# Performance work log

Hardware: AMD Instinct MI355X
Metric: run time of the kernel (lower is better)

The kernel has to match this reference:

```python
import jax, jax.numpy as jnp
import numpy as np

IN_FEATURES = 512
DIM_EXPLOSION = 20
OUT_FEATURES = IN_FEATURES * DIM_EXPLOSION  # 10240
NB_PROJ_ENTRIES = 6
HASH_LENGTH = 32
BATCH = 4096


def _make_sparse_proj(key):
    """Sparse binary random projection: each of the OUT_FEATURES rows has
    NB_PROJ_ENTRIES entries set to 1 (as in OlfactoryModel.create_rand_proj_matrix)."""
    idx = jax.random.randint(key, (OUT_FEATURES, NB_PROJ_ENTRIES), 0, IN_FEATURES)
    rows = jnp.arange(OUT_FEATURES)[:, None]
    W = jnp.zeros((OUT_FEATURES, IN_FEATURES), dtype=jnp.float32)
    return W.at[rows, idx].set(1.0)


def setup_inputs() -> dict:
    key = jax.random.key(0)
    k1, k2 = jax.random.split(key)
    inp = jax.random.uniform(k1, (BATCH, IN_FEATURES), dtype=jnp.float32)
    W = _make_sparse_proj(k2)
    return {"input": inp, "weight": W, "hash_length": HASH_LENGTH}


def reference(input, weight, hash_length):
    # F.linear: [B, in] @ [out, in]^T -> [B, out]
    x = jnp.einsum('bi,oi->bo', input, weight)
    # MB_sparsify: winner-take-all, keep top `hash_length` activations per row, zero the rest
    topv = jax.lax.top_k(x, hash_length)[0]          # [B, k]
    thresh = topv[:, -1:]                            # k-th largest per row
    return jnp.where(x >= thresh, x, jnp.zeros_like(x))
```

## Files before the change

kernel.cpp:

```cpp
#include <hip/hip_runtime.h>


typedef float f4 __attribute__((ext_vector_type(4)));

constexpr int IN_F   = 512;
constexpr int OUT_F  = 10240;
constexpr int TPB    = 1024;
constexpr int ROWS   = 4;
constexpr int FPT    = OUT_F / TPB;
constexpr int NBINS  = 1024;
constexpr int CHUNK  = 8;
constexpr int NCHUNK = NBINS / CHUNK;
constexpr int NWAVES = TPB / 64;
constexpr int CAP    = 64;

__global__ __launch_bounds__(256) void extract_idx(const float* __restrict__ W,
                                                   uint4* __restrict__ packed,
                                                   int out_f) {
  int row  = blockIdx.x * 4 + (threadIdx.x >> 6);
  int lane = threadIdx.x & 63;
  if (row >= out_f) return;

  const float* wr = W + (size_t)row * IN_F;
  unsigned long long masks[8];
#pragma unroll
  for (int c = 0; c < 8; ++c) {
    float v = wr[c * 64 + lane];
    masks[c] = __ballot(v != 0.0f);
  }
  if (lane == 0) {
    unsigned idx[6] = {IN_F, IN_F, IN_F, IN_F, IN_F, IN_F};
    int n = 0;
#pragma unroll
    for (int c = 0; c < 8; ++c) {
      unsigned long long m = masks[c];
      while (m && n < 6) {
        int b = __builtin_ctzll(m);
        idx[n++] = (unsigned)(c * 64 + b);
        m &= m - 1;
      }
    }
    uint4 r;
    r.x = idx[0] | (idx[1] << 16);
    r.y = idx[2] | (idx[3] << 16);
    r.z = idx[4] | (idx[5] << 16);
    r.w = (unsigned)n;
    packed[row] = r;
  }
}

__global__ __launch_bounds__(TPB, 8) void fly_hash(const float* __restrict__ inp,
                                                   const uint4* __restrict__ packed,
                                                   const int* __restrict__ kptr,
                                                   float* __restrict__ out) {
  __shared__ f4    in4[IN_F + 1];
  __shared__ int   hist[ROWS * NBINS];
  __shared__ int   csum[ROWS * NCHUNK];
  __shared__ int   wsum[NWAVES][ROWS];
  __shared__ int   sh_bstar[ROWS], sh_above[ROWS], sh_n[ROWS], sh_cnt[ROWS];
  __shared__ float sh_list[ROWS][CAP];
  __shared__ float sh_thr[ROWS];
  __shared__ int   sh_need[ROWS];

  const int tid  = threadIdx.x;
  const int row0 = blockIdx.x * ROWS;
  const int k    = *kptr;

  if (tid < IN_F) {
    const float* p = inp + (size_t)row0 * IN_F + tid;
    f4 v;
    v.x = p[0];
    v.y = p[IN_F];
    v.z = p[2 * IN_F];
    v.w = p[3 * IN_F];
    in4[tid] = v;
  }
  if (tid == 0) { f4 z = {0.0f, 0.0f, 0.0f, 0.0f}; in4[IN_F] = z; }
  if (tid < ROWS) { sh_bstar[tid] = -1; sh_cnt[tid] = 0; }
  for (int i = tid; i < ROWS * NBINS; i += TPB) hist[i] = 0;
  __syncthreads();

  f4 x4[FPT];
#pragma unroll
  for (int i = 0; i < FPT; ++i) {
    uint4 r = packed[tid + i * TPB];
    f4 s = in4[r.x & 0xFFFFu];
    s += in4[r.x >> 16];
    s += in4[r.y & 0xFFFFu];
    s += in4[r.y >> 16];
    s += in4[r.z & 0xFFFFu];
    s += in4[r.z >> 16];
    x4[i] = s;
#pragma unroll
    for (int r2 = 0; r2 < ROWS; ++r2) {
      float v = (r2 == 0) ? s.x : (r2 == 1) ? s.y : (r2 == 2) ? s.z : s.w;
      if (v >= 4.0f) {
        int b = (int)((v - 4.0f) * 512.0f);
        b = b > NBINS - 1 ? NBINS - 1 : b;
        atomicAdd(&hist[r2 * NBINS + b], 1);
      }
    }
  }
  __syncthreads();

  {
    const bool active = tid < ROWS * NCHUNK;
    const int r = tid >> 7;
    const int c = tid & (NCHUNK - 1);
    if (active) {
      const int base = r * NBINS + c * CHUNK;
      int ssum = 0;
#pragma unroll
      for (int j = 0; j < CHUNK; ++j) ssum += hist[base + j];
      csum[tid] = ssum;
    }
    __syncthreads();
    for (int st = 1; st < NCHUNK; st <<= 1) {
      int v = 0;
      if (active) v = csum[tid] + ((c + st < NCHUNK) ? csum[tid + st] : 0);
      __syncthreads();
      if (active) csum[tid] = v;
      __syncthreads();
    }
    if (active) {
      int above_chunk = (c + 1 < NCHUNK) ? csum[tid + 1] : 0;
      if (csum[tid] >= k && above_chunk < k) {
        int acc = above_chunk;
        int bsel = c * CHUNK, abv = above_chunk;
        for (int b = c * CHUNK + CHUNK - 1; b >= c * CHUNK; --b) {
          int h = hist[r * NBINS + b];
          if (acc + h >= k) { bsel = b; abv = acc; break; }
          acc += h;
        }
        sh_bstar[r] = bsel;
        sh_above[r] = abv;
        sh_n[r]     = hist[r * NBINS + bsel];
      }
    }
  }
  __syncthreads();

  {
    const int b0 = sh_bstar[0], b1 = sh_bstar[1];
    const int b2 = sh_bstar[2], b3 = sh_bstar[3];
#pragma unroll
    for (int i = 0; i < FPT; ++i) {
      f4 s = x4[i];
#pragma unroll
      for (int r2 = 0; r2 < ROWS; ++r2) {
        float v = (r2 == 0) ? s.x : (r2 == 1) ? s.y : (r2 == 2) ? s.z : s.w;
        int bb = (r2 == 0) ? b0 : (r2 == 1) ? b1 : (r2 == 2) ? b2 : b3;
        if (v >= 4.0f) {
          int b = (int)((v - 4.0f) * 512.0f);
          b = b > NBINS - 1 ? NBINS - 1 : b;
          if (b == bb) {
            int p = atomicAdd(&sh_cnt[r2], 1);
            if (p < CAP) sh_list[r2][p] = v;
          }
        }
      }
    }
  }
  __syncthreads();

  {
    const int wid  = tid >> 6;
    const int lane = tid & 63;
    if (wid < ROWS) {
      const int r = wid;
      const int bst = sh_bstar[r];
      const int n   = (bst >= 0) ? sh_n[r] : CAP + 1;
      if (bst >= 0 && n <= CAP) {
        const int j = k - sh_above[r];
        float vl = (lane < n) ? sh_list[r][lane] : -1.0f;
        int c_gt = 0, c_ge = 0;
        for (int m = 0; m < n; ++m) {
          float u = sh_list[r][m];
          c_gt += (u > vl);
          c_ge += (u >= vl);
        }
        if (lane < n && c_gt < j && c_ge >= j) sh_thr[r] = vl;
        if (lane == 0) sh_need[r] = 0;
      } else {
        if (lane == 0) sh_need[r] = 1;
      }
    }
  }
  __syncthreads();

  unsigned lo[ROWS], hi[ROWS];
#pragma unroll
  for (int r = 0; r < ROWS; ++r) {
    if (sh_need[r]) {
      int b = sh_bstar[r];
      if (b < 0) {
        lo[r] = 0u;
        hi[r] = __float_as_uint(4.0f + (1.0f / 512.0f));
      } else {
        lo[r] = __float_as_uint(4.0f + (float)b * (1.0f / 512.0f));
        hi[r] = __float_as_uint(4.0f + (float)(b + 1) * (1.0f / 512.0f));
      }
    } else {
      lo[r] = hi[r] = 0u;
    }
  }
  {
    const int lane = tid & 63;
    const int wid  = tid >> 6;
    while (lo[0] < hi[0] || lo[1] < hi[1] || lo[2] < hi[2] || lo[3] < hi[3]) {
      unsigned mid[ROWS];
      float fm[ROWS];
#pragma unroll
      for (int r = 0; r < ROWS; ++r) {
        mid[r] = lo[r] + ((hi[r] - lo[r] + 1u) >> 1);
        fm[r] = __uint_as_float(mid[r]);
      }
      int c0 = 0, c1 = 0, c2 = 0, c3 = 0;
#pragma unroll
      for (int i = 0; i < FPT; ++i) {
        c0 += (int)__popcll(__ballot(x4[i].x >= fm[0]));
        c1 += (int)__popcll(__ballot(x4[i].y >= fm[1]));
        c2 += (int)__popcll(__ballot(x4[i].z >= fm[2]));
        c3 += (int)__popcll(__ballot(x4[i].w >= fm[3]));
      }
      if (lane == 0) {
        wsum[wid][0] = c0; wsum[wid][1] = c1;
        wsum[wid][2] = c2; wsum[wid][3] = c3;
      }
      __syncthreads();
      int tot[ROWS] = {0, 0, 0, 0};
#pragma unroll
      for (int w = 0; w < NWAVES; ++w)
#pragma unroll
        for (int r = 0; r < ROWS; ++r) tot[r] += wsum[w][r];
#pragma unroll
      for (int r = 0; r < ROWS; ++r) {
        if (lo[r] < hi[r]) {
          if (tot[r] >= k) lo[r] = mid[r]; else hi[r] = mid[r] - 1u;
        }
      }
      __syncthreads();
    }
  }
  const float t0 = sh_need[0] ? __uint_as_float(lo[0]) : sh_thr[0];
  const float t1 = sh_need[1] ? __uint_as_float(lo[1]) : sh_thr[1];
  const float t2 = sh_need[2] ? __uint_as_float(lo[2]) : sh_thr[2];
  const float t3 = sh_need[3] ? __uint_as_float(lo[3]) : sh_thr[3];

  float* o0 = out + (size_t)(row0 + 0) * OUT_F;
  float* o1 = out + (size_t)(row0 + 1) * OUT_F;
  float* o2 = out + (size_t)(row0 + 2) * OUT_F;
  float* o3 = out + (size_t)(row0 + 3) * OUT_F;
#pragma unroll
  for (int i = 0; i < FPT; ++i) {
    int f = tid + i * TPB;
    f4 v = x4[i];
    __builtin_nontemporal_store((v.x >= t0) ? v.x : 0.0f, &o0[f]);
    __builtin_nontemporal_store((v.y >= t1) ? v.y : 0.0f, &o1[f]);
    __builtin_nontemporal_store((v.z >= t2) ? v.z : 0.0f, &o2[f]);
    __builtin_nontemporal_store((v.w >= t3) ? v.w : 0.0f, &o3[f]);
  }
}

extern "C" void kernel_launch(void* const* d_in, const int* in_sizes, int n_in,
                              void* d_out, int out_size, void* d_ws, size_t ws_size,
                              hipStream_t stream) {
  const float* inp = (const float*)d_in[0];
  const float* W   = (const float*)d_in[1];
  const int* kptr  = (const int*)d_in[2];
  float* out       = (float*)d_out;

  const int batch = in_sizes[0] / IN_F;
  const int out_f = in_sizes[1] / IN_F;

  uint4* packed = (uint4*)d_ws;

  hipLaunchKernelGGL(extract_idx, dim3((out_f + 3) / 4), dim3(256), 0, stream,
                     W, packed, out_f);
  hipLaunchKernelGGL(fly_hash, dim3(batch / ROWS), dim3(TPB), 0, stream,
                     inp, packed, kptr, out);
}
```

Baseline: 279.7 us.

## Drop register-resident activations; zero output and scatter only candidate winners

Stops keeping all 40 activations per thread in registers. Each block zero-fills its output rows up front, and values at or above 4.0 are compacted into a per-row shared-memory candidate list with wave-aggregated atomics. The threshold is found from the histogram bin plus that list, and only candidates are scattered back to the output. The goal is lower register pressure and higher occupancy. In exchange, shared memory grows by roughly 40KB, the zero-fill and scatter write the output twice, and the fallback path recomputes the projection from global indices for a full-range bisection.

```diff
diff --git a/kernel.cpp b/kernel.cpp
--- a/kernel.cpp
+++ b/kernel.cpp
@@ -12,7 +12,8 @@
 constexpr int CHUNK  = 8;
 constexpr int NCHUNK = NBINS / CHUNK;
 constexpr int NWAVES = TPB / 64;
-constexpr int CAP    = 64;
+constexpr int CAP    = 1280;
+constexpr int MCAP   = 64;
 
 __global__ __launch_bounds__(256) void extract_idx(const float* __restrict__ W,
                                                    uint4* __restrict__ packed,
@@ -47,6 +48,17 @@
     r.w = (unsigned)n;
     packed[row] = r;
   }
+}
+
+__device__ __forceinline__ float row_val(const f4* in4, uint4 p, int r) {
+  const float* b = (const float*)in4;
+  float s = b[(p.x & 0xFFFFu) * 4 + r];
+  s += b[(p.x >> 16) * 4 + r];
+  s += b[(p.y & 0xFFFFu) * 4 + r];
+  s += b[(p.y >> 16) * 4 + r];
+  s += b[(p.z & 0xFFFFu) * 4 + r];
+  s += b[(p.z >> 16) * 4 + r];
+  return s;
 }
 
 __global__ __launch_bounds__(TPB, 8) void fly_hash(const float* __restrict__ inp,
@@ -56,15 +68,19 @@
   __shared__ f4    in4[IN_F + 1];
   __shared__ int   hist[ROWS * NBINS];
   __shared__ int   csum[ROWS * NCHUNK];
-  __shared__ int   wsum[NWAVES][ROWS];
+  __shared__ int   wsum[NWAVES];
+  __shared__ uint2 cand[ROWS][CAP];
+  __shared__ float mem[ROWS][MCAP];
   __shared__ int   sh_bstar[ROWS], sh_above[ROWS], sh_n[ROWS], sh_cnt[ROWS];
-  __shared__ float sh_list[ROWS][CAP];
   __shared__ float sh_thr[ROWS];
   __shared__ int   sh_need[ROWS];
 
   const int tid  = threadIdx.x;
+  const int lane = tid & 63;
+  const int wid  = tid >> 6;
   const int row0 = blockIdx.x * ROWS;
   const int k    = *kptr;
+  float* const obase = out + (size_t)row0 * OUT_F;
 
   if (tid < IN_F) {
     const float* p = inp + (size_t)row0 * IN_F + tid;
@@ -74,30 +90,46 @@
     v.z = p[2 * IN_F];
     v.w = p[3 * IN_F];
     in4[tid] = v;
-  }
-  if (tid == 0) { f4 z = {0.0f, 0.0f, 0.0f, 0.0f}; in4[IN_F] = z; }
+  } else if (tid == IN_F) {
+    f4 z = {0.0f, 0.0f, 0.0f, 0.0f};
+    in4[IN_F] = z;
+  }
   if (tid < ROWS) { sh_bstar[tid] = -1; sh_cnt[tid] = 0; }
   for (int i = tid; i < ROWS * NBINS; i += TPB) hist[i] = 0;
-  __syncthreads();
-
-  f4 x4[FPT];
-#pragma unroll
+  {
+    f4 z = {0.0f, 0.0f, 0.0f, 0.0f};
+    f4* oz = (f4*)obase;
+#pragma unroll
+    for (int j = 0; j < FPT; ++j) oz[tid + j * TPB] = z;
+  }
+  __syncthreads();
+
+#pragma unroll 2
   for (int i = 0; i < FPT; ++i) {
-    uint4 r = packed[tid + i * TPB];
+    const int f = tid + i * TPB;
+    uint4 r = packed[f];
     f4 s = in4[r.x & 0xFFFFu];
     s += in4[r.x >> 16];
     s += in4[r.y & 0xFFFFu];
     s += in4[r.y >> 16];
     s += in4[r.z & 0xFFFFu];
     s += in4[r.z >> 16];
-    x4[i] = s;
-#pragma unroll
-    for (int r2 = 0; r2 < ROWS; ++r2) {
-      float v = (r2 == 0) ? s.x : (r2 == 1) ? s.y : (r2 == 2) ? s.z : s.w;
-      if (v >= 4.0f) {
-        int b = (int)((v - 4.0f) * 512.0f);
-        b = b > NBINS - 1 ? NBINS - 1 : b;
-        atomicAdd(&hist[r2 * NBINS + b], 1);
+#pragma unroll
+    for (int rr = 0; rr < ROWS; ++rr) {
+      float v = s[rr];
+      unsigned long long m = __ballot(v >= 4.0f);
+      if (m) {
+        int lead = __ffsll(m) - 1;
+        int base = 0;
+        if (lane == lead) base = atomicAdd(&sh_cnt[rr], (int)__popcll(m));
+        base = __shfl(base, lead);
+        if (v >= 4.0f) {
+          int slot = base + (int)__popcll(m & ((1ull << lane) - 1ull));
+          if (slot < CAP) cand[rr][slot] = make_uint2((unsigned)f, __float_as_uint(v));
+          int b = (int)((v - 4.0f) * 512.0f);
+          b = b > NBINS - 1 ? NBINS - 1 : b;
+          atomicAdd(&hist[rr * NBINS + b], 1);
+        }
       }
     }
   }
@@ -140,125 +172,85 @@
   }
   __syncthreads();
 
-  {
-    const int b0 = sh_bstar[0], b1 = sh_bstar[1];
-    const int b2 = sh_bstar[2], b3 = sh_bstar[3];
-#pragma unroll
+  if (wid < ROWS) {
+    const int r   = wid;
+    const int bst = sh_bstar[r];
+    const int cnt = sh_cnt[r];
+    bool ok = (bst >= 0) && (cnt <= CAP);
+    const int n = ok ? sh_n[r] : 0;
+    ok = ok && (n >= 1) && (n <= MCAP);
+    if (ok) {
+      int nm = 0;
+      for (int base = 0; base < cnt; base += 64) {
+        int idx = base + lane;
+        bool act = idx < cnt;
+        uint2 e = act ? cand[r][idx] : make_uint2(0u, 0u);
+        float v = __uint_as_float(e.y);
+        int b = (int)((v - 4.0f) * 512.0f);
+        b = b > NBINS - 1 ? NBINS - 1 : b;
+        bool ism = act && (b == bst);
+        unsigned long long m = __ballot(ism);
+        if (ism) {
+          int ofs = nm + (int)__popcll(m & ((1ull << lane) - 1ull));
+          if (ofs < MCAP) mem[r][ofs] = v;
+        }
+        nm += (int)__popcll(m);
+      }
+      const int j = k - sh_above[r];
+      float vl = (lane < n) ? mem[r][lane] : -1.0f;
+      int cgt = 0, cge = 0;
+      for (int mi = 0; mi < n; ++mi) {
+        float u = mem[r][mi];
+        cgt += (u > vl);
+        cge += (u >= vl);
+      }
+      if (lane < n && cgt < j && cge >= j) sh_thr[r] = vl;
+      if (lane == 0) sh_need[r] = 0;
+    } else {
+      if (lane == 0) sh_need[r] = 1;
+    }
+  }
+  __syncthreads();
+
+#pragma unroll 1
+  for (int r = 0; r < ROWS; ++r) {
+    if (!sh_need[r]) continue;
+    unsigned lo = 0u, hi = __float_as_uint(8.0f);
+    while (lo < hi) {
+      unsigned mid = lo + ((hi - lo + 1u) >> 1);
+      float fm = __uint_as_float(mid);
+      int c = 0;
+      for (int i = 0; i < FPT; ++i) {
+        uint4 p = packed[tid + i * TPB];
+        c += (int)__popcll(__ballot(row_val(in4, p, r) >= fm));
+      }
+      if (lane == 0) wsum[wid] = c;
+      __syncthreads();
+      int tot = 0;
+#pragma unroll
+      for (int w = 0; w < NWAVES; ++w) tot += wsum[w];
+      if (tot >= k) lo = mid; else hi = mid - 1u;
+      __syncthreads();
+    }
+    float thr = __uint_as_float(lo);
     for (int i = 0; i < FPT; ++i) {
-      f4 s = x4[i];
-#pragma unroll
-      for (int r2 = 0; r2 < ROWS; ++r2) {
-        float v = (r2 == 0) ? s.x : (r2 == 1) ? s.y : (r2 == 2) ? s.z : s.w;
-        int bb = (r2 == 0) ? b0 : (r2 == 1) ? b1 : (r2 == 2) ? b2 : b3;
-        if (v >= 4.0f) {
-          int b = (int)((v - 4.0f) * 512.0f);
-          b = b > NBINS - 1 ? NBINS - 1 : b;
-          if (b == bb) {
-            int p = atomicAdd(&sh_cnt[r2], 1);
-            if (p < CAP) sh_list[r2][p] = v;
-          }
-        }
-      }
-    }
-  }
-  __syncthreads();
-
-  {
-    const int wid  = tid >> 6;
-    const int lane = tid & 63;
-    if (wid < ROWS) {
-      const int r = wid;
-      const int bst = sh_bstar[r];
-      const int n   = (bst >= 0) ? sh_n[r] : CAP + 1;
-      if (bst >= 0 && n <= CAP) {
-        const int j = k - sh_above[r];
-        float vl = (lane < n) ? sh_list[r][lane] : -1.0f;
-        int c_gt = 0, c_ge = 0;
-        for (int m = 0; m < n; ++m) {
-          float u = sh_list[r][m];
-          c_gt += (u > vl);
-          c_ge += (u >= vl);
-        }
-        if (lane < n && c_gt < j && c_ge >= j) sh_thr[r] = vl;
-        if (lane == 0) sh_need[r] = 0;
-      } else {
-        if (lane == 0) sh_need[r] = 1;
-      }
-    }
-  }
-  __syncthreads();
-
-  unsigned lo[ROWS], hi[ROWS];
+      int f = tid + i * TPB;
+      float v = row_val(in4, packed[f], r);
+      obase[(size_t)r * OUT_F + f] = (v >= thr) ? v : 0.0f;
+    }
+  }
+
 #pragma unroll
   for (int r = 0; r < ROWS; ++r) {
-    if (sh_need[r]) {
-      int b = sh_bstar[r];
-      if (b < 0) {
-        lo[r] = 0u;
-        hi[r] = __float_as_uint(4.0f + (1.0f / 512.0f));
-      } else {
-        lo[r] = __float_as_uint(4.0f + (float)b * (1.0f / 512.0f));
-        hi[r] = __float_as_uint(4.0f + (float)(b + 1) * (1.0f / 512.0f));
-      }
-    } else {
-      lo[r] = hi[r] = 0u;
-    }
-  }
-  {
-    const int lane = tid & 63;
-    const int wid  = tid >> 6;
-    while (lo[0] < hi[0] || lo[1] < hi[1] || lo[2] < hi[2] || lo[3] < hi[3]) {
-      unsigned mid[ROWS];
-      float fm[ROWS];
-#pragma unroll
-      for (int r = 0; r < ROWS; ++r) {
-        mid[r] = lo[r] + ((hi[r] - lo[r] + 1u) >> 1);
-        fm[r] = __uint_as_float(mid[r]);
-      }
-      int c0 = 0, c1 = 0, c2 = 0, c3 = 0;
-#pragma unroll
-      for (int i = 0; i < FPT; ++i) {
-        c0 += (int)__popcll(__ballot(x4[i].x >= fm[0]));
-        c1 += (int)__popcll(__ballot(x4[i].y >= fm[1]));
-        c2 += (int)__popcll(__ballot(x4[i].z >= fm[2]));
-        c3 += (int)__popcll(__ballot(x4[i].w >= fm[3]));
-      }
-      if (lane == 0) {
-        wsum[wid][0] = c0; wsum[wid][1] = c1;
-        wsum[wid][2] = c2; wsum[wid][3] = c3;
-      }
-      __syncthreads();
-      int tot[ROWS] = {0, 0, 0, 0};
-#pragma unroll
-      for (int w = 0; w < NWAVES; ++w)
-#pragma unroll
-        for (int r = 0; r < ROWS; ++r) tot[r] += wsum[w][r];
-#pragma unroll
-      for (int r = 0; r < ROWS; ++r) {
-        if (lo[r] < hi[r]) {
-          if (tot[r] >= k) lo[r] = mid[r]; else hi[r] = mid[r] - 1u;
-        }
-      }
-      __syncthreads();
-    }
-  }
-  const float t0 = sh_need[0] ? __uint_as_float(lo[0]) : sh_thr[0];
-  const float t1 = sh_need[1] ? __uint_as_float(lo[1]) : sh_thr[1];
-  const float t2 = sh_need[2] ? __uint_as_float(lo[2]) : sh_thr[2];
-  const float t3 = sh_need[3] ? __uint_as_float(lo[3]) : sh_thr[3];
-
-  float* o0 = out + (size_t)(row0 + 0) * OUT_F;
-  float* o1 = out + (size_t)(row0 + 1) * OUT_F;
-  float* o2 = out + (size_t)(row0 + 2) * OUT_F;
-  float* o3 = out + (size_t)(row0 + 3) * OUT_F;
-#pragma unroll
-  for (int i = 0; i < FPT; ++i) {
-    int f = tid + i * TPB;
-    f4 v = x4[i];
-    __builtin_nontemporal_store((v.x >= t0) ? v.x : 0.0f, &o0[f]);
-    __builtin_nontemporal_store((v.y >= t1) ? v.y : 0.0f, &o1[f]);
-    __builtin_nontemporal_store((v.z >= t2) ? v.z : 0.0f, &o2[f]);
-    __builtin_nontemporal_store((v.w >= t3) ? v.w : 0.0f, &o3[f]);
+    if (sh_need[r]) continue;
+    const int cn = sh_cnt[r];
+    const float tr = sh_thr[r];
+    float* orow = obase + (size_t)r * OUT_F;
+    for (int idx = tid; idx < cn; idx += TPB) {
+      uint2 e = cand[r][idx];
+      float v = __uint_as_float(e.y);
+      orow[e.x] = (v >= tr) ? v : 0.0f;
+    }
   }
 }
 
```

New measurement: 484.9 us. 73.4% more time.
